# Kernel optimization log

Hardware: AMD Instinct MI355X
Metric: run time of the kernel (lower is better)

The kernel has to match this reference:

```python
import jax, jax.numpy as jnp
import numpy as np

WIN = 11  # hard-coded window size in the original module

def sinusoidal_pe(L, D):
    pos = jnp.arange(L, dtype=jnp.float32)[:, None]
    div = jnp.exp(jnp.arange(0, D, 2, dtype=jnp.float32) * (-np.log(10000.0) / D))
    pe = jnp.zeros((L, D), dtype=jnp.float32)
    pe = pe.at[:, 0::2].set(jnp.sin(pos * div))
    pe = pe.at[:, 1::2].set(jnp.cos(pos * div))
    return pe


def setup_inputs() -> dict:
    key = jax.random.key(0)
    ks = jax.random.split(key, 6)
    B, Lq, Ld, D, V = 16, 30, 1100, 768, 50000
    return {
        "q": jax.random.randint(ks[0], (B, Lq), 0, V),
        "d_pos": jax.random.randint(ks[1], (B, Ld), 0, V),
        "d_neg": jax.random.randint(ks[2], (B, Ld), 0, V),
        "q_mask": jnp.ones((B, Lq, 1), jnp.float32),
        "d_pos_mask": jnp.ones((B, Ld, 1), jnp.float32),
        "d_neg_mask": jnp.ones((B, Ld, 1), jnp.float32),
        "pe_flag": 1,
        "emb_table": jax.random.normal(ks[3], (V, D), jnp.float32) * 0.02,
        "W_lin": jax.random.normal(ks[4], (D, D), jnp.float32) * 0.02,
        "W_out": jax.random.normal(ks[5], (D, D), jnp.float32) * 0.02,
    }


def reference(q, d_pos, d_neg, q_mask, d_pos_mask, d_neg_mask, pe_flag, emb_table, W_lin, W_out):
    B, Lq = q.shape
    Ld = d_pos.shape[1]
    D = emb_table.shape[1]
    H = 12
    Dh = D // H
    W_num = Ld // WIN  # number of 11-token windows

    qe = emb_table[q] * q_mask              # [B,Lq,D]
    dp = emb_table[d_pos]                   # [B,Ld,D]
    dn = emb_table[d_neg]
    if pe_flag:
        pe = sinusoidal_pe(Ld, D)[None]     # [1,Ld,D]
        scale_emb = jnp.sqrt(jnp.float32(D))
        dp = dp * scale_emb + pe            # dropout p=0 -> identity
        dn = dn * scale_emb + pe
    dp = dp * d_pos_mask
    dn = dn * d_neg_mask

    dp = dp.reshape(B, W_num, WIN, D)       # [B,W,11,D]
    dn = dn.reshape(B, W_num, WIN, D)
    qx = jnp.broadcast_to(qe[:, None], (B, W_num, Lq, D))  # expand over windows

    # linear_trans (no bias): y = x @ W_lin.T
    queries = jnp.einsum('bwqd,ed->bwqe', qx, W_lin)
    dp = jnp.einsum('bwkd,ed->bwke', dp, W_lin)
    dn = jnp.einsum('bwkd,ed->bwke', dn, W_lin)

    # faithful replication of torch .view head-split: pure reshape, mixes seq+channel
    def split(x, L):
        return x.reshape(B, W_num, H, L, Dh)

    queries = split(queries, Lq) * (Dh ** -0.5)

    def attend(doc):
        d = split(doc, WIN)                                  # [B,W,H,11,Dh]
        logits = jnp.einsum('bwhqd,bwhkd->bwhqk', queries, d)
        weights = jax.nn.softmax(logits, axis=-1)            # dropout p=0
        ctx = jnp.einsum('bwhqk,bwhkd->bwhqd', weights, d)
        ctx = ctx.reshape(B, W_num, Lq, D)                   # faithful merge (.view)
        return jnp.einsum('bwqd,ed->bwqe', ctx, W_out)

    return attend(dp), attend(dn)
```

## Files before the change

kernel.cpp:

```cpp
#include <hip/hip_runtime.h>
#include <hip/hip_bf16.h>
#include <cstdint>
#include <cstddef>

#define B_    16
#define LQ    30
#define LD    1100
#define DIM   768
#define NH    12
#define DH_   64
#define WINSZ 11
#define WNUM  100
#define NSLOT 32

typedef __attribute__((ext_vector_type(8))) short short8;
typedef __attribute__((ext_vector_type(4))) float f32x4;

__device__ __forceinline__ void gload_lds16(const void* g, void* l) {
  __builtin_amdgcn_global_load_lds(
      (const __attribute__((address_space(1))) void*)g,
      (__attribute__((address_space(3))) void*)l, 16, 0, 0);
}

__global__ __launch_bounds__(256) void wconv_kernel(const float* __restrict__ wa,
    const float* __restrict__ wb, __hip_bfloat16* __restrict__ oa,
    __hip_bfloat16* __restrict__ ob) {
  int i = (blockIdx.x * 256 + threadIdx.x) * 4;
  if (i >= DIM * DIM) return;
  float4 va = *reinterpret_cast<const float4*>(wa + i);
  float4 vb = *reinterpret_cast<const float4*>(wb + i);
  union { __hip_bfloat16 h[4]; uint2 u; } pa, pb;
  pa.h[0] = __float2bfloat16(va.x); pa.h[1] = __float2bfloat16(va.y);
  pa.h[2] = __float2bfloat16(va.z); pa.h[3] = __float2bfloat16(va.w);
  pb.h[0] = __float2bfloat16(vb.x); pb.h[1] = __float2bfloat16(vb.y);
  pb.h[2] = __float2bfloat16(vb.z); pb.h[3] = __float2bfloat16(vb.w);
  *reinterpret_cast<uint2*>(oa + i) = pa.u;
  *reinterpret_cast<uint2*>(ob + i) = pb.u;
}

__global__ __launch_bounds__(256) void pe_kernel(float* __restrict__ pe) {
  int idx = blockIdx.x * 256 + threadIdx.x;
  if (idx >= LD * (DIM / 4)) return;
  int t  = idx / (DIM / 4);
  int c4 = idx % (DIM / 4);
  int i0 = c4 * 2;
  float d0 = expf(-0.023985261387f * (float)i0);
  float d1 = expf(-0.023985261387f * (float)(i0 + 1));
  float s0f, c0f, s1f, c1f;
  sincosf((float)t * d0, &s0f, &c0f);
  sincosf((float)t * d1, &s1f, &c1f);
  *reinterpret_cast<float4*>(pe + (size_t)t * DIM + c4 * 4) =
      make_float4(s0f, c0f, s1f, c1f);
}

__global__ __launch_bounds__(256) void prep_q_kernel(const int* __restrict__ q,
    const float* __restrict__ qmask, const float* __restrict__ emb,
    __hip_bfloat16* __restrict__ Xq) {
  int idx = blockIdx.x * 256 + threadIdx.x;
  if (idx >= B_ * LQ * (DIM / 4)) return;
  int row = idx / (DIM / 4);
  int c4  = idx % (DIM / 4);
  float m = qmask[row] * 0.125f;
  float4 v = *reinterpret_cast<const float4*>(emb + (size_t)q[row] * DIM + c4 * 4);
  union { __hip_bfloat16 h[4]; uint2 u; } o;
  o.h[0] = __float2bfloat16(v.x * m); o.h[1] = __float2bfloat16(v.y * m);
  o.h[2] = __float2bfloat16(v.z * m); o.h[3] = __float2bfloat16(v.w * m);
  *reinterpret_cast<uint2*>(Xq + (size_t)row * DIM + c4 * 4) = o.u;
}

__global__ __launch_bounds__(256) void prep_d_kernel(const int* __restrict__ dpos,
    const int* __restrict__ dneg, const float* __restrict__ dpmask,
    const float* __restrict__ dnmask, const float* __restrict__ emb,
    const int* __restrict__ peflag, const float* __restrict__ pe,
    __hip_bfloat16* __restrict__ X, int s0, int rows) {
  int idx = blockIdx.x * 256 + threadIdx.x;
  if (idx >= rows * (DIM / 4)) return;
  int r  = idx / (DIM / 4);
  int c4 = idx % (DIM / 4);
  int s = s0 + r / LD;
  int t = r % LD;
  int doc = s >> 4, b = s & 15;
  const int*   di = doc ? dneg   : dpos;
  const float* dm = doc ? dnmask : dpmask;
  int grow = b * LD + t;
  float m = dm[grow];
  float4 v = *reinterpret_cast<const float4*>(emb + (size_t)di[grow] * DIM + c4 * 4);
  if (peflag[0]) {
    float4 p = *reinterpret_cast<const float4*>(pe + (size_t)t * DIM + c4 * 4);
    v.x = v.x * 27.712812921102035f + p.x;
    v.y = v.y * 27.712812921102035f + p.y;
    v.z = v.z * 27.712812921102035f + p.z;
    v.w = v.w * 27.712812921102035f + p.w;
  }
  union { __hip_bfloat16 h[4]; uint2 u; } o;
  o.h[0] = __float2bfloat16(v.x * m); o.h[1] = __float2bfloat16(v.y * m);
  o.h[2] = __float2bfloat16(v.z * m); o.h[3] = __float2bfloat16(v.w * m);
  *reinterpret_cast<uint2*>(X + (size_t)r * DIM + c4 * 4) = o.u;
}

template <bool OUT_BF16>
__global__ __launch_bounds__(512, 2) void gemm_mfma(const __hip_bfloat16* __restrict__ A,
    const __hip_bfloat16* __restrict__ Bt, void* __restrict__ Cv,
    int M, int N, int K, int tilesX, int tiles1,
    const __hip_bfloat16* __restrict__ A2, float* __restrict__ C2, int M2) {
  extern __shared__ __hip_bfloat16 smem[];
  __hip_bfloat16* As = smem;
  __hip_bfloat16* Bs = smem + 4 * 8192;

  const int nwg  = gridDim.x;
  const int orig = blockIdx.x;
  const int q8 = nwg >> 3, r8 = nwg & 7;
  const int xcd = orig & 7, pos = orig >> 3;
  const int wgid = (xcd < r8 ? xcd * (q8 + 1) : r8 * (q8 + 1) + (xcd - r8) * q8) + pos;

  const bool is2 = (wgid >= tiles1);
  const int  w2  = is2 ? (wgid - tiles1) : wgid;
  const int row0 = (w2 / tilesX) * 256;
  const int col0 = (w2 % tilesX) * 256;
  const __hip_bfloat16* Ap = is2 ? A2 : A;
  const int Mloc = is2 ? M2 : M;

  const int tid  = threadIdx.x;
  const int lane = tid & 63;
  const int wave = tid >> 6;
  const int wr = wave >> 2, wc = wave & 3;
  const int lo4 = lane & 15;
  const int hi4 = lane >> 4;

  const int csrc = (tid & 3) ^ ((tid >> 3) & 3);
  const __hip_bfloat16* gA = Ap + (size_t)(row0 + (tid >> 2)) * K + csrc * 8;
  const __hip_bfloat16* gB = Bt + (size_t)(col0 + (tid >> 2)) * K + csrc * 8;

  const int coff = ((hi4 ^ ((lo4 >> 1) & 3)) * 8);
  const int arow = (wr * 128 + lo4) * 32 + coff;
  const int brow = (wc * 64  + lo4) * 32 + coff;

  f32x4 acc[8][4] = {};

  auto STAGE = [&](int tt) {
    const int k0 = tt * 32;
    const int lo = (tt & 3) * 8192;
    gload_lds16(gA + k0,                   As + lo + tid * 8);
    gload_lds16(gA + (size_t)128 * K + k0, As + lo + 4096 + tid * 8);
    gload_lds16(gB + k0,                   Bs + lo + tid * 8);
    gload_lds16(gB + (size_t)128 * K + k0, Bs + lo + 4096 + tid * 8);
  };

#define MFMA4(MB)                                                       \
    _Pragma("unroll")                                                   \
    for (int n = 0; n < 4; ++n)                                         \
      acc[MB][n] = __builtin_amdgcn_mfma_f32_16x16x32_bf16(             \
          bq[n], af0, acc[MB][n], 0, 0, 0);                             \
    _Pragma("unroll")                                                   \
    for (int n = 0; n < 4; ++n)                                         \
      acc[MB + 1][n] = __builtin_amdgcn_mfma_f32_16x16x32_bf16(         \
          bq[n], af1, acc[MB + 1][n], 0, 0, 0);

#define STEP(tt, WAITN, DOSTAGE)                                        \
  {                                                                     \
    const int lo = ((tt) & 3) * 8192;                                   \
    const int so = (((tt) + 3) & 3) * 8192;                             \
    const int k0s = ((tt) + 3) * 32;                                    \
    const __hip_bfloat16* Ab = As + lo + arow;                          \
    const __hip_bfloat16* Bb = Bs + lo + brow;                          \
    short8 bq[4], af0, af1, af2, af3;                                   \
                                                 \
    asm volatile("s_waitcnt vmcnt(" WAITN ")" ::: "memory");            \
    __builtin_amdgcn_s_barrier();                                       \
    __builtin_amdgcn_sched_barrier(0);                                  \
    bq[0] = *reinterpret_cast<const short8*>(Bb);                       \
    bq[1] = *reinterpret_cast<const short8*>(Bb + 512);                 \
    bq[2] = *reinterpret_cast<const short8*>(Bb + 1024);                \
    bq[3] = *reinterpret_cast<const short8*>(Bb + 1536);                \
    af0 = *reinterpret_cast<const short8*>(Ab);                         \
    af1 = *reinterpret_cast<const short8*>(Ab + 512);                   \
    af2 = *reinterpret_cast<const short8*>(Ab + 1024);                  \
    af3 = *reinterpret_cast<const short8*>(Ab + 1536);                  \
    if (DOSTAGE) {                                                      \
      gload_lds16(gA + k0s,                   As + so + tid * 8);       \
      gload_lds16(gA + (size_t)128 * K + k0s, As + so + 4096 + tid * 8);\
    }                                                                   \
    asm volatile("s_waitcnt lgkmcnt(0)" ::: "memory");                  \
    __builtin_amdgcn_sched_barrier(0);                                  \
    __builtin_amdgcn_s_setprio(1);                                      \
    MFMA4(0)                                                            \
    { short8 t0 = af2, t1 = af3; af0 = t0; af1 = t1; }                  \
    MFMA4(2)                                                            \
    __builtin_amdgcn_s_setprio(0);                                      \
                                                 \
    __builtin_amdgcn_s_barrier();                                       \
    af0 = *reinterpret_cast<const short8*>(Ab + 2048);                  \
    af1 = *reinterpret_cast<const short8*>(Ab + 2560);                  \
    af2 = *reinterpret_cast<const short8*>(Ab + 3072);                  \
    af3 = *reinterpret_cast<const short8*>(Ab + 3584);                  \
    if (DOSTAGE) {                                                      \
      gload_lds16(gB + k0s,                   Bs + so + tid * 8);       \
      gload_lds16(gB + (size_t)128 * K + k0s, Bs + so + 4096 + tid * 8);\
    }                                                                   \
    asm volatile("s_waitcnt lgkmcnt(0)" ::: "memory");                  \
    __builtin_amdgcn_sched_barrier(0);                                  \
    __builtin_amdgcn_s_setprio(1);                                      \
    MFMA4(4)                                                            \
    { short8 t0 = af2, t1 = af3; af0 = t0; af1 = t1; }                  \
    MFMA4(6)                                                            \
    __builtin_amdgcn_s_setprio(0);                                      \
  }

  const int nt = K / 32;
  STAGE(0); STAGE(1); STAGE(2);
  for (int t = 0; t < nt - 3; ++t)
    STEP(t, "8", true)
  STEP(nt - 3, "8", false)
  STEP(nt - 2, "4", false)
  STEP(nt - 1, "0", false)
#undef STEP
#undef MFMA4

#pragma unroll
  for (int m = 0; m < 8; ++m) {
    const int r = row0 + wr * 128 + m * 16 + lo4;
    if (r < Mloc) {
#pragma unroll
      for (int n = 0; n < 4; ++n) {
        const int cb = col0 + wc * 64 + n * 16 + hi4 * 4;
        f32x4 v = acc[m][n];
        if (is2) {
          *reinterpret_cast<f32x4*>(C2 + (size_t)r * N + cb) = v;
        } else if constexpr (OUT_BF16) {
          union { __hip_bfloat16 h[4]; uint2 u; } p;
          p.h[0] = __float2bfloat16(v[0]); p.h[1] = __float2bfloat16(v[1]);
          p.h[2] = __float2bfloat16(v[2]); p.h[3] = __float2bfloat16(v[3]);
          *reinterpret_cast<uint2*>((__hip_bfloat16*)Cv + (size_t)r * N + cb) = p.u;
        } else {
          __builtin_nontemporal_store(
              v, reinterpret_cast<f32x4*>((float*)Cv + (size_t)r * N + cb));
        }
      }
    }
  }
}

__global__ __launch_bounds__(128) void attn_kernel(const float* __restrict__ Qs,
    const __hip_bfloat16* __restrict__ Y, __hip_bfloat16* __restrict__ ctx, int s0) {
  int blk = blockIdx.x;
  int h  = blk % NH;
  int w  = (blk / NH) % WNUM;
  int sl = blk / (NH * WNUM);
  int b  = (s0 + sl) & 15;

  __shared__ float Dl[WINSZ][DH_];

  const __hip_bfloat16* Yb = Y + ((size_t)(sl * LD + w * WINSZ)) * DIM + h * (WINSZ * DH_);
  const float* Qb = Qs + (size_t)b * (LQ * DIM) + h * (LQ * DH_);

  int tid = threadIdx.x;
  int qi = tid >> 2, part = tid & 3;

  if (tid < 88) {
    uint4 raw = *reinterpret_cast<const uint4*>(Yb + tid * 8);
    const __hip_bfloat16* hp = reinterpret_cast<const __hip_bfloat16*>(&raw);
    float* dst = &Dl[0][0] + tid * 8;
#pragma unroll
    for (int j = 0; j < 8; ++j) dst[j] = __bfloat162float(hp[j]);
  }

  float4 qreg[4];
#pragma unroll
  for (int j = 0; j < 4; ++j)
    qreg[j] = *reinterpret_cast<const float4*>(Qb + qi * DH_ + part * 16 + j * 4);
  __syncthreads();

  float dot[WINSZ];
#pragma unroll
  for (int k = 0; k < WINSZ; ++k) {
    const float4* dp = reinterpret_cast<const float4*>(&Dl[k][part * 16]);
    float s = 0.f;
#pragma unroll
    for (int j = 0; j < 4; ++j) {
      float4 dv = dp[j];
      s += qreg[j].x * dv.x + qreg[j].y * dv.y + qreg[j].z * dv.z + qreg[j].w * dv.w;
    }
    dot[k] = s;
  }
#pragma unroll
  for (int k = 0; k < WINSZ; ++k) {
    dot[k] += __shfl_xor(dot[k], 1);
    dot[k] += __shfl_xor(dot[k], 2);
  }
  float mx = -1e30f;
#pragma unroll
  for (int k = 0; k < WINSZ; ++k) mx = fmaxf(mx, dot[k]);
  float sum = 0.f;
#pragma unroll
  for (int k = 0; k < WINSZ; ++k) { dot[k] = expf(dot[k] - mx); sum += dot[k]; }
  float inv = 1.f / sum;

  float4 o[4] = {};
#pragma unroll
  for (int k = 0; k < WINSZ; ++k) {
    float pk = dot[k];
    const float4* dp = reinterpret_cast<const float4*>(&Dl[k][part * 16]);
#pragma unroll
    for (int j = 0; j < 4; ++j) {
      float4 dv = dp[j];
      o[j].x += pk * dv.x; o[j].y += pk * dv.y;
      o[j].z += pk * dv.z; o[j].w += pk * dv.w;
    }
  }
  union { __hip_bfloat16 hh[16]; uint4 v[2]; } pk;
#pragma unroll
  for (int j = 0; j < 4; ++j) {
    pk.hh[j * 4 + 0] = __float2bfloat16(o[j].x * inv);
    pk.hh[j * 4 + 1] = __float2bfloat16(o[j].y * inv);
    pk.hh[j * 4 + 2] = __float2bfloat16(o[j].z * inv);
    pk.hh[j * 4 + 3] = __float2bfloat16(o[j].w * inv);
  }
  __hip_bfloat16* op = ctx + (size_t)(sl * WNUM + w) * (LQ * DIM)
                     + h * (LQ * DH_) + qi * DH_ + part * 16;
  *reinterpret_cast<uint4*>(op)     = pk.v[0];
  *reinterpret_cast<uint4*>(op + 8) = pk.v[1];
}

extern "C" void kernel_launch(void* const* d_in, const int* in_sizes, int n_in,
                              void* d_out, int out_size, void* d_ws, size_t ws_size,
                              hipStream_t stream) {
  const int*   q      = (const int*)d_in[0];
  const int*   dpos   = (const int*)d_in[1];
  const int*   dneg   = (const int*)d_in[2];
  const float* qmask  = (const float*)d_in[3];
  const float* dpmask = (const float*)d_in[4];
  const float* dnmask = (const float*)d_in[5];
  const int*   peflag = (const int*)d_in[6];
  const float* emb    = (const float*)d_in[7];
  const float* Wlin   = (const float*)d_in[8];
  const float* Wout   = (const float*)d_in[9];
  float* out = (float*)d_out;

  (void)hipFuncSetAttribute(reinterpret_cast<const void*>(&gemm_mfma<false>),
                            hipFuncAttributeMaxDynamicSharedMemorySize, 131072);
  (void)hipFuncSetAttribute(reinterpret_cast<const void*>(&gemm_mfma<true>),
                            hipFuncAttributeMaxDynamicSharedMemorySize, 131072);

  char* ws = (char*)d_ws;
  size_t off = 0;
  auto alloc = [&](size_t bytes) -> char* {
    char* p = ws + off; off += (bytes + 255) & ~(size_t)255; return p;
  };
  __hip_bfloat16* Xq   = (__hip_bfloat16*)alloc((size_t)512 * DIM * 2);
  float*          Qsc  = (float*)         alloc((size_t)B_ * LQ * DIM * 4);
  __hip_bfloat16* Wl16 = (__hip_bfloat16*)alloc((size_t)DIM * DIM * 2);
  __hip_bfloat16* Wo16 = (__hip_bfloat16*)alloc((size_t)DIM * DIM * 2);
  float*          PE   = (float*)         alloc((size_t)LD * DIM * 4);

  int SC = NSLOT;
  while (SC > 1) {
    size_t need = off
        + ((size_t)SC * LD + 256) * DIM * 2 * 2
        + ((size_t)SC * WNUM * LQ + 256) * DIM * 2 + (1u << 20);
    if (need <= ws_size) break;
    SC >>= 1;
  }
  __hip_bfloat16* X   = (__hip_bfloat16*)alloc(((size_t)SC * LD + 256) * DIM * 2);
  __hip_bfloat16* Y   = (__hip_bfloat16*)alloc(((size_t)SC * LD + 256) * DIM * 2);
  __hip_bfloat16* ctx = (__hip_bfloat16*)alloc(((size_t)SC * WNUM * LQ + 256) * DIM * 2);

  wconv_kernel<<<(DIM * DIM / 4 + 255) / 256, 256, 0, stream>>>(Wlin, Wout, Wl16, Wo16);
  pe_kernel<<<(LD * (DIM / 4) + 255) / 256, 256, 0, stream>>>(PE);
  prep_q_kernel<<<(B_ * LQ * (DIM / 4) + 255) / 256, 256, 0, stream>>>(q, qmask, emb, Xq);

  const int tilesX = DIM / 256;
  const int qTiles = tilesX * ((B_ * LQ + 255) / 256);

  for (int s0 = 0; s0 < NSLOT; s0 += SC) {
    const int rowsX = SC * LD;
    const int rowsC = SC * WNUM * LQ;
    prep_d_kernel<<<(rowsX * (DIM / 4) + 255) / 256, 256, 0, stream>>>(
        dpos, dneg, dpmask, dnmask, emb, peflag, PE, X, s0, rowsX);
    {
      int tiles1 = tilesX * ((rowsX + 255) / 256);
      int t2 = (s0 == 0) ? qTiles : 0;
      gemm_mfma<true><<<tiles1 + t2, 512, 131072, stream>>>(
          X, Wl16, Y, rowsX, DIM, DIM, tilesX, tiles1, Xq, Qsc, B_ * LQ);
    }
    attn_kernel<<<SC * WNUM * NH, 120, 0, stream>>>(Qsc, Y, ctx, s0);
    {
      int tiles1 = tilesX * ((rowsC + 255) / 256);
      gemm_mfma<false><<<tiles1, 512, 131072, stream>>>(
          ctx, Wo16, out + (size_t)s0 * WNUM * LQ * DIM, rowsC, DIM, DIM,
          tilesX, tiles1, nullptr, nullptr, 0);
    }
  }
}
```

Baseline: 392.7 us.

## Restructure GEMM main loop to K=64 double-buffered stages with finer interleaving

```diff
diff --git a/kernel.cpp b/kernel.cpp
--- a/kernel.cpp
+++ b/kernel.cpp
@@ -104,8 +104,6 @@
     int M, int N, int K, int tilesX, int tiles1,
     const __hip_bfloat16* __restrict__ A2, float* __restrict__ C2, int M2) {
   extern __shared__ __hip_bfloat16 smem[];
-  __hip_bfloat16* As = smem;
-  __hip_bfloat16* Bs = smem + 4 * 8192;
 
   const int nwg  = gridDim.x;
   const int orig = blockIdx.x;
@@ -127,94 +125,132 @@
   const int lo4 = lane & 15;
   const int hi4 = lane >> 4;
 
-  const int csrc = (tid & 3) ^ ((tid >> 3) & 3);
-  const __hip_bfloat16* gA = Ap + (size_t)(row0 + (tid >> 2)) * K + csrc * 8;
-  const __hip_bfloat16* gB = Bt + (size_t)(col0 + (tid >> 2)) * K + csrc * 8;
-
-  const int coff = ((hi4 ^ ((lo4 >> 1) & 3)) * 8);
-  const int arow = (wr * 128 + lo4) * 32 + coff;
-  const int brow = (wc * 64  + lo4) * 32 + coff;
+  const int u0 = tid,        r0s = u0 >> 3, x0s = u0 & 7;
+  const int u1 = 512 + tid,  r1s = u1 >> 3, x1s = u1 & 7;
+  const int soff0 = r0s * K + ((x0s ^ (r0s & 7)) * 8);
+  const int soff1 = r1s * K + ((x1s ^ (r1s & 7)) * 8);
+  const int wvoff = wave * 512;
+  const __hip_bfloat16* gA = Ap + (size_t)row0 * K;
+  const __hip_bfloat16* gB = Bt + (size_t)col0 * K;
+
+#define STAGE_HALF(PTR, KOFF, HALF, SLOTBASE)                            \
+  gload_lds16((PTR) + (size_t)(HALF) * (128 * 768) + (KOFF) + soff0,    \
+              smem + (SLOTBASE) + (HALF) * 8192 + wvoff);               \
+  gload_lds16((PTR) + (size_t)(HALF) * (128 * 768) + (KOFF) + soff1,    \
+              smem + (SLOTBASE) + (HALF) * 8192 + 4096 + wvoff);
+
+  const int rA = (wr * 128 + lo4) * 64;
+  const int rB = (wc * 64  + lo4) * 64;
+  const int xk0 = ((0 + hi4) ^ (lo4 & 7)) * 8;
+  const int xk1 = ((4 + hi4) ^ (lo4 & 7)) * 8;
+
+#define LDA(S, MM, XK) (*reinterpret_cast<const short8*>(smem + (S) * 16384 + rA + (MM) * 1024 + (XK)))
+#define LDB(S, NN, XK) (*reinterpret_cast<const short8*>(smem + 32768 + (S) * 16384 + rB + (NN) * 1024 + (XK)))
 
   f32x4 acc[8][4] = {};
-
-  auto STAGE = [&](int tt) {
-    const int k0 = tt * 32;
-    const int lo = (tt & 3) * 8192;
-    gload_lds16(gA + k0,                   As + lo + tid * 8);
-    gload_lds16(gA + (size_t)128 * K + k0, As + lo + 4096 + tid * 8);
-    gload_lds16(gB + k0,                   Bs + lo + tid * 8);
-    gload_lds16(gB + (size_t)128 * K + k0, Bs + lo + 4096 + tid * 8);
-  };
-
-#define MFMA4(MB)                                                       \
-    _Pragma("unroll")                                                   \
-    for (int n = 0; n < 4; ++n)                                         \
-      acc[MB][n] = __builtin_amdgcn_mfma_f32_16x16x32_bf16(             \
-          bq[n], af0, acc[MB][n], 0, 0, 0);                             \
-    _Pragma("unroll")                                                   \
-    for (int n = 0; n < 4; ++n)                                         \
-      acc[MB + 1][n] = __builtin_amdgcn_mfma_f32_16x16x32_bf16(         \
-          bq[n], af1, acc[MB + 1][n], 0, 0, 0);
-
-#define STEP(tt, WAITN, DOSTAGE)                                        \
-  {                                                                     \
-    const int lo = ((tt) & 3) * 8192;                                   \
-    const int so = (((tt) + 3) & 3) * 8192;                             \
-    const int k0s = ((tt) + 3) * 32;                                    \
-    const __hip_bfloat16* Ab = As + lo + arow;                          \
-    const __hip_bfloat16* Bb = Bs + lo + brow;                          \
-    short8 bq[4], af0, af1, af2, af3;                                   \
-                                                 \
-    asm volatile("s_waitcnt vmcnt(" WAITN ")" ::: "memory");            \
-    __builtin_amdgcn_s_barrier();                                       \
-    __builtin_amdgcn_sched_barrier(0);                                  \
-    bq[0] = *reinterpret_cast<const short8*>(Bb);                       \
-    bq[1] = *reinterpret_cast<const short8*>(Bb + 512);                 \
-    bq[2] = *reinterpret_cast<const short8*>(Bb + 1024);                \
-    bq[3] = *reinterpret_cast<const short8*>(Bb + 1536);                \
-    af0 = *reinterpret_cast<const short8*>(Ab);                         \
-    af1 = *reinterpret_cast<const short8*>(Ab + 512);                   \
-    af2 = *reinterpret_cast<const short8*>(Ab + 1024);                  \
-    af3 = *reinterpret_cast<const short8*>(Ab + 1536);                  \
-    if (DOSTAGE) {                                                      \
-      gload_lds16(gA + k0s,                   As + so + tid * 8);       \
-      gload_lds16(gA + (size_t)128 * K + k0s, As + so + 4096 + tid * 8);\
-    }                                                                   \
-    asm volatile("s_waitcnt lgkmcnt(0)" ::: "memory");                  \
-    __builtin_amdgcn_sched_barrier(0);                                  \
-    __builtin_amdgcn_s_setprio(1);                                      \
-    MFMA4(0)                                                            \
-    { short8 t0 = af2, t1 = af3; af0 = t0; af1 = t1; }                  \
-    MFMA4(2)                                                            \
-    __builtin_amdgcn_s_setprio(0);                                      \
-                                                 \
-    __builtin_amdgcn_s_barrier();                                       \
-    af0 = *reinterpret_cast<const short8*>(Ab + 2048);                  \
-    af1 = *reinterpret_cast<const short8*>(Ab + 2560);                  \
-    af2 = *reinterpret_cast<const short8*>(Ab + 3072);                  \
-    af3 = *reinterpret_cast<const short8*>(Ab + 3584);                  \
-    if (DOSTAGE) {                                                      \
-      gload_lds16(gB + k0s,                   Bs + so + tid * 8);       \
-      gload_lds16(gB + (size_t)128 * K + k0s, Bs + so + 4096 + tid * 8);\
-    }                                                                   \
-    asm volatile("s_waitcnt lgkmcnt(0)" ::: "memory");                  \
-    __builtin_amdgcn_sched_barrier(0);                                  \
-    __builtin_amdgcn_s_setprio(1);                                      \
-    MFMA4(4)                                                            \
-    { short8 t0 = af2, t1 = af3; af0 = t0; af1 = t1; }                  \
-    MFMA4(6)                                                            \
-    __builtin_amdgcn_s_setprio(0);                                      \
-  }
-
-  const int nt = K / 32;
-  STAGE(0); STAGE(1); STAGE(2);
-  for (int t = 0; t < nt - 3; ++t)
-    STEP(t, "8", true)
-  STEP(nt - 3, "8", false)
-  STEP(nt - 2, "4", false)
-  STEP(nt - 1, "0", false)
-#undef STEP
-#undef MFMA4
+  short8 bf[4][2], aa0, aa1, aa2, aa3;
+
+#define MM4(MMI, KK, AREG)                                                         \
+  acc[MMI][0] = __builtin_amdgcn_mfma_f32_16x16x32_bf16(bf[0][KK], AREG, acc[MMI][0], 0, 0, 0); \
+  acc[MMI][1] = __builtin_amdgcn_mfma_f32_16x16x32_bf16(bf[1][KK], AREG, acc[MMI][1], 0, 0, 0); \
+  acc[MMI][2] = __builtin_amdgcn_mfma_f32_16x16x32_bf16(bf[2][KK], AREG, acc[MMI][2], 0, 0, 0); \
+  acc[MMI][3] = __builtin_amdgcn_mfma_f32_16x16x32_bf16(bf[3][KK], AREG, acc[MMI][3], 0, 0, 0);
+#define MFMA_PAIR(MA, MB) MM4(MA, 0, aa0) MM4(MB, 0, aa1) MM4(MA, 1, aa2) MM4(MB, 1, aa3)
+
+#define LDB8(S)                                                          \
+  bf[0][0] = LDB(S, 0, xk0); bf[1][0] = LDB(S, 1, xk0);                  \
+  bf[2][0] = LDB(S, 2, xk0); bf[3][0] = LDB(S, 3, xk0);                  \
+  bf[0][1] = LDB(S, 0, xk1); bf[1][1] = LDB(S, 1, xk1);                  \
+  bf[2][1] = LDB(S, 2, xk1); bf[3][1] = LDB(S, 3, xk1);
+#define LDA4(S, MA, MB)                                                  \
+  aa0 = LDA(S, MA, xk0); aa1 = LDA(S, MB, xk0);                          \
+  aa2 = LDA(S, MA, xk1); aa3 = LDA(S, MB, xk1);
+
+#define BARR  { __builtin_amdgcn_s_barrier(); __builtin_amdgcn_sched_barrier(0); }
+#define VMW(NLIT) asm volatile("s_waitcnt vmcnt(" NLIT ")" ::: "memory");
+#define SYNC_MFMA { asm volatile("s_waitcnt lgkmcnt(0)" ::: "memory");   \
+                    __builtin_amdgcn_sched_barrier(0);                   \
+                    __builtin_amdgcn_s_setprio(1); }
+#define END_MFMA  __builtin_amdgcn_s_setprio(0);
+
+  STAGE_HALF(gB, 0,   0, 32768) STAGE_HALF(gB, 0,   1, 32768)
+  STAGE_HALF(gA, 0,   0, 0)     STAGE_HALF(gA, 0,   1, 0)
+  STAGE_HALF(gB, 64,  0, 49152) STAGE_HALF(gB, 64,  1, 49152)
+
+  for (int it = 0; it < 5; ++it) {
+    const int kb = it * 128;
+    VMW("4") BARR
+    LDB8(0) LDA4(0, 0, 1)
+    STAGE_HALF(gA, kb + 64, 0, 16384)
+    SYNC_MFMA MFMA_PAIR(0, 1) END_MFMA
+    BARR
+    LDA4(0, 2, 3)
+    STAGE_HALF(gA, kb + 64, 1, 16384)
+    SYNC_MFMA MFMA_PAIR(2, 3) END_MFMA
+    BARR
+    LDA4(0, 4, 5)
+    STAGE_HALF(gB, kb + 128, 0, 32768)
+    SYNC_MFMA MFMA_PAIR(4, 5) END_MFMA
+    BARR
+    LDA4(0, 6, 7)
+    STAGE_HALF(gB, kb + 128, 1, 32768)
+    SYNC_MFMA MFMA_PAIR(6, 7) END_MFMA
+    VMW("4") BARR
+    LDB8(1) LDA4(1, 0, 1)
+    STAGE_HALF(gA, kb + 128, 0, 0)
+    SYNC_MFMA MFMA_PAIR(0, 1) END_MFMA
+    BARR
+    LDA4(1, 2, 3)
+    STAGE_HALF(gA, kb + 128, 1, 0)
+    SYNC_MFMA MFMA_PAIR(2, 3) END_MFMA
+    BARR
+    LDA4(1, 4, 5)
+    STAGE_HALF(gB, kb + 192, 0, 49152)
+    SYNC_MFMA MFMA_PAIR(4, 5) END_MFMA
+    BARR
+    LDA4(1, 6, 7)
+    STAGE_HALF(gB, kb + 192, 1, 49152)
+    SYNC_MFMA MFMA_PAIR(6, 7) END_MFMA
+  }
+
+  VMW("4") BARR
+  LDB8(0) LDA4(0, 0, 1)
+  STAGE_HALF(gA, 704, 0, 16384)
+  SYNC_MFMA MFMA_PAIR(0, 1) END_MFMA
+  BARR
+  LDA4(0, 2, 3)
+  STAGE_HALF(gA, 704, 1, 16384)
+  SYNC_MFMA MFMA_PAIR(2, 3) END_MFMA
+  BARR
+  LDA4(0, 4, 5)
+  SYNC_MFMA MFMA_PAIR(4, 5) END_MFMA
+  BARR
+  LDA4(0, 6, 7)
+  SYNC_MFMA MFMA_PAIR(6, 7) END_MFMA
+  VMW("0") BARR
+  LDB8(1) LDA4(1, 0, 1)
+  SYNC_MFMA MFMA_PAIR(0, 1) END_MFMA
+  BARR
+  LDA4(1, 2, 3)
+  SYNC_MFMA MFMA_PAIR(2, 3) END_MFMA
+  BARR
+  LDA4(1, 4, 5)
+  SYNC_MFMA MFMA_PAIR(4, 5) END_MFMA
+  BARR
+  LDA4(1, 6, 7)
+  SYNC_MFMA MFMA_PAIR(6, 7) END_MFMA
+
+#undef STAGE_HALF
+#undef LDA
+#undef LDB
+#undef MM4
+#undef MFMA_PAIR
+#undef LDB8
+#undef LDA4
+#undef BARR
+#undef VMW
+#undef SYNC_MFMA
+#undef END_MFMA
 
 #pragma unroll
   for (int m = 0; m < 8; ++m) {
```

Result: faster. 374.4 us (-4.7%).
